# Optimization experiments

Measured on AMD Instinct MI355X. Metric: run time of the kernel, lower is better.

The kernel has to match this reference:

```python
import jax, jax.numpy as jnp
import numpy as np

EMB = 1024
HID = 2048
HEADS = 16
CONV = 4


def causal_conv1d(z, w):
    # z: [B, H, T], w: [H, K] depthwise causal conv
    K = w.shape[1]
    T = z.shape[-1]
    zp = jnp.pad(z, ((0, 0), (0, 0), (K - 1, 0)))  # [B, H, T+K-1]
    out = jnp.zeros_like(z)
    for k in range(K):  # tiny fixed loop over taps (K<=4)
        out = out + w[None, :, k, None] * jax.lax.dynamic_slice_in_dim(zp, k, T, axis=2)
    return out


def linear_scan(a, b):
    # h_t = a_t * h_{t-1} + b_t along last axis; associative scan
    def combine(c1, c2):
        a1, b1 = c1
        a2, b2 = c2
        return a1 * a2, a2 * b1 + b2
    _, h = jax.lax.associative_scan(combine, (a, b), axis=-1)
    return h


def setup_inputs() -> dict:
    key = jax.random.key(0)
    k1, k2, k3, k4 = jax.random.split(key, 4)
    x = jax.random.normal(k1, (4, 2048, EMB), dtype=jnp.float32)
    w1 = jax.random.normal(k2, (3 * HID, EMB), dtype=jnp.float32) * (EMB ** -0.5)
    w2 = jax.random.normal(k3, (EMB, HID), dtype=jnp.float32) * (HID ** -0.5)
    conv_weight = jax.random.normal(k4, (HID, CONV), dtype=jnp.float32) * (CONV ** -0.5)
    return {"x": x, "w1": w1, "w2": w2, "conv_weight": conv_weight}


def reference(x, w1, w2, conv_weight):
    bsz, seq_len, _ = x.shape
    head_dim = HID // HEADS
    y = jnp.einsum("bse,he->bsh", x, w1)  # [B, S, 3*HID]
    out1, z, h = jnp.split(y, 3, axis=-1)
    z = jnp.swapaxes(z, 1, 2)  # [B, HID, S]
    h = jnp.swapaxes(h, 1, 2)
    z = causal_conv1d(z, conv_weight)
    z = jax.nn.sigmoid(z)
    z = z.reshape(bsz * HEADS, head_dim, seq_len)
    h = h.reshape(bsz * HEADS, head_dim, seq_len)
    h = linear_scan(1.0 - z, z * h)
    out2 = jnp.swapaxes(h.reshape(bsz, HID, seq_len), 1, 2)  # [B, S, HID]
    out = jax.nn.silu(out1) * out2
    return jnp.einsum("bsh,eh->bse", out, w2)
```

## Files before the change

kernel.cpp:

```cpp
#include <hip/hip_runtime.h>
#include <cstdint>

#define EMB 1024
#define HID 2048
#define BATCH 4
#define SEQ 2048
#define MROWS (BATCH * SEQ)
#define N1 (3 * HID)
#define K1 EMB
#define N2 EMB
#define K2 HID

#define NX (MROWS * EMB)
#define NW1 (N1 * K1)
#define NW2 (N2 * K2)

#define SEG 32
#define SLEN (SEQ / SEG)

typedef unsigned short ushort_t;
typedef __bf16 bf16x8 __attribute__((ext_vector_type(8)));
typedef float f32x4 __attribute__((ext_vector_type(4)));
typedef ushort_t us4 __attribute__((ext_vector_type(4)));

__device__ __forceinline__ ushort_t f2bf(float f) {
    uint32_t u = __builtin_bit_cast(uint32_t, f);
    u += 0x7fffu + ((u >> 16) & 1u);
    return (ushort_t)(u >> 16);
}
__device__ __forceinline__ float bf2f(ushort_t h) {
    uint32_t u = ((uint32_t)h) << 16;
    return __builtin_bit_cast(float, u);
}
__device__ __forceinline__ float bflo(uint32_t v) {
    return __builtin_bit_cast(float, v << 16);
}
__device__ __forceinline__ float bfhi(uint32_t v) {
    return __builtin_bit_cast(float, v & 0xffff0000u);
}
__device__ __forceinline__ float sigm(float x) {
    return 1.f / (1.f + __expf(-x));
}

__device__ __forceinline__ void gload_lds16(const ushort_t* g, const ushort_t* l) {
    __builtin_amdgcn_global_load_lds(
        (const __attribute__((address_space(1))) void*)(uintptr_t)(g),
        (__attribute__((address_space(3))) void*)(uint32_t)(uintptr_t)(l),
        16, 0, 0);
}

__global__ __launch_bounds__(256) void cvt_kernel(
    const float* __restrict__ x, const float* __restrict__ w1,
    const float* __restrict__ w2, ushort_t* __restrict__ xb,
    ushort_t* __restrict__ w1b, ushort_t* __restrict__ w2b) {
    const int i = (blockIdx.x * 256 + threadIdx.x) * 4;
    const float* s;
    ushort_t* d;
    if (i < NX) {
        s = x + i; d = xb + i;
    } else if (i < NX + NW1) {
        s = w1 + (i - NX); d = w1b + (i - NX);
    } else {
        s = w2 + (i - NX - NW1); d = w2b + (i - NX - NW1);
    }
    const float4 v = *(const float4*)s;
    us4 o;
    o.x = f2bf(v.x); o.y = f2bf(v.y); o.z = f2bf(v.z); o.w = f2bf(v.w);
    *(us4*)d = o;
}

template <bool OUT_BF16>
__global__ __launch_bounds__(256) void gemm_bt(
    const ushort_t* __restrict__ A, const ushort_t* __restrict__ B,
    void* __restrict__ Cv, int M, int N, int K) {
    __shared__ ushort_t sA[128 * 32];
    __shared__ ushort_t sB[128 * 32];

    const int tid  = threadIdx.x;
    const int lane = tid & 63;
    const int wave = tid >> 6;
    const int quad = lane >> 4;
    const int l16  = lane & 15;
    const long tm0 = (long)blockIdx.y * 128;
    const long tn0 = (long)blockIdx.x * 128;
    const int wm = (wave & 1) * 64;
    const int wn = (wave >> 1) * 64;

    f32x4 acc[4][4] = {};

    const int ar0 = tid >> 2;
    const int ar1 = (tid + 256) >> 2;
    const int kq  = (tid & 3) ^ ((ar0 >> 1) & 3);
    const int ac  = kq * 8;
    const ushort_t* gA = A + (size_t)tm0 * K;
    const ushort_t* gB = B + (size_t)tn0 * K;
    ushort_t* lb0 = &sA[0] + wave * 512;
    ushort_t* lb1 = &sA[0] + 2048 + wave * 512;
    ushort_t* lb2 = &sB[0] + wave * 512;
    ushort_t* lb3 = &sB[0] + 2048 + wave * 512;

    const int rsw = (l16 >> 1) & 3;
    const int aoff = (quad ^ rsw) * 8 + l16 * 32;

    for (int k0 = 0; k0 < K; k0 += 32) {
        __syncthreads();
        gload_lds16(gA + (size_t)ar0 * K + k0 + ac, lb0);
        gload_lds16(gA + (size_t)ar1 * K + k0 + ac, lb1);
        gload_lds16(gB + (size_t)ar0 * K + k0 + ac, lb2);
        gload_lds16(gB + (size_t)ar1 * K + k0 + ac, lb3);
        __syncthreads();

        bf16x8 af[4], bfr[4];
#pragma unroll
        for (int i = 0; i < 4; ++i)
            af[i] = *(const bf16x8*)&sA[(wm + i * 16) * 32 + aoff];
#pragma unroll
        for (int j = 0; j < 4; ++j)
            bfr[j] = *(const bf16x8*)&sB[(wn + j * 16) * 32 + aoff];
#pragma unroll
        for (int i = 0; i < 4; ++i)
#pragma unroll
            for (int j = 0; j < 4; ++j)
                acc[i][j] = __builtin_amdgcn_mfma_f32_16x16x32_bf16(
                    af[i], bfr[j], acc[i][j], 0, 0, 0);
    }

#pragma unroll
    for (int i = 0; i < 4; ++i) {
        const long row0 = tm0 + wm + i * 16 + quad * 4;
#pragma unroll
        for (int j = 0; j < 4; ++j) {
            const long col = tn0 + wn + j * 16 + l16;
#pragma unroll
            for (int r = 0; r < 4; ++r) {
                if constexpr (OUT_BF16) {
                    ((ushort_t*)Cv)[(size_t)(row0 + r) * N + col] = f2bf(acc[i][j][r]);
                } else {
                    ((float*)Cv)[(size_t)(row0 + r) * N + col] = acc[i][j][r];
                }
            }
        }
    }
}

__global__ __launch_bounds__(256) void scan_part1(
    const ushort_t* __restrict__ y, const float* __restrict__ cw,
    float* __restrict__ Ag, float* __restrict__ Bg) {
    const int gid = blockIdx.x * 256 + threadIdx.x;
    const int ch  = (gid & 1023) * 2;
    const int bs  = gid >> 10;
    const int b   = bs >> 5;
    const int seg = bs & 31;
    const int t0  = seg * SLEN;
    const size_t rowbase = (size_t)b * SEQ;
    const ushort_t* yz = y + 2048 + ch;
    const ushort_t* yh = y + 4096 + ch;

    float w[2][4];
#pragma unroll
    for (int c = 0; c < 2; ++c)
#pragma unroll
        for (int k = 0; k < 4; ++k) w[c][k] = cw[(ch + c) * 4 + k];

    auto ld2 = [&](const ushort_t* p, int t) -> uint32_t {
        return *(const uint32_t*)(p + (rowbase + (size_t)t) * 6144);
    };
    auto zpair = [&](int t, float* out) {
        if (t < 0) { out[0] = 0.f; out[1] = 0.f; }
        else { uint32_t v = ld2(yz, t); out[0] = bflo(v); out[1] = bfhi(v); }
    };

    float z1[2], z2[2], z3[2], A[2] = {1.f, 1.f}, Bv[2] = {0.f, 0.f};
    zpair(t0 - 1, z1); zpair(t0 - 2, z2); zpair(t0 - 3, z3);

#pragma unroll 4
    for (int t = t0; t < t0 + SLEN; ++t) {
        const uint32_t vz = ld2(yz, t);
        const uint32_t vh = ld2(yh, t);
        const float zr[2] = {bflo(vz), bfhi(vz)};
        const float hr[2] = {bflo(vh), bfhi(vh)};
#pragma unroll
        for (int c = 0; c < 2; ++c) {
            const float cv = w[c][0] * z3[c] + w[c][1] * z2[c] +
                             w[c][2] * z1[c] + w[c][3] * zr[c];
            const float s = sigm(cv);
            z3[c] = z2[c]; z2[c] = z1[c]; z1[c] = zr[c];
            const float a = 1.f - s;
            A[c] *= a;
            Bv[c] = a * Bv[c] + s * hr[c];
        }
    }
    const size_t idx = ((size_t)b * SEG + seg) * HID + ch;
    *(float2*)&Ag[idx] = make_float2(A[0], A[1]);
    *(float2*)&Bg[idx] = make_float2(Bv[0], Bv[1]);
}

__global__ __launch_bounds__(256) void scan_part2(
    const float* __restrict__ Ag, const float* __restrict__ Bg,
    float* __restrict__ Cr) {
    const int gid = blockIdx.x * 256 + threadIdx.x;
    const int b  = gid >> 11;
    const int ch = gid & 2047;
    float carry = 0.f;
#pragma unroll
    for (int s = 0; s < SEG; ++s) {
        const size_t idx = ((size_t)b * SEG + s) * HID + ch;
        Cr[idx] = carry;
        carry = Ag[idx] * carry + Bg[idx];
    }
}

__global__ __launch_bounds__(256) void scan_part3(
    const ushort_t* __restrict__ y, const float* __restrict__ cw,
    const float* __restrict__ Cr, ushort_t* __restrict__ u) {
    const int gid = blockIdx.x * 256 + threadIdx.x;
    const int ch  = (gid & 1023) * 2;
    const int bs  = gid >> 10;
    const int b   = bs >> 5;
    const int seg = bs & 31;
    const int t0  = seg * SLEN;
    const size_t rowbase = (size_t)b * SEQ;
    const ushort_t* yo = y + ch;
    const ushort_t* yz = y + 2048 + ch;
    const ushort_t* yh = y + 4096 + ch;

    float w[2][4];
#pragma unroll
    for (int c = 0; c < 2; ++c)
#pragma unroll
        for (int k = 0; k < 4; ++k) w[c][k] = cw[(ch + c) * 4 + k];

    auto ld2 = [&](const ushort_t* p, int t) -> uint32_t {
        return *(const uint32_t*)(p + (rowbase + (size_t)t) * 6144);
    };
    auto zpair = [&](int t, float* out) {
        if (t < 0) { out[0] = 0.f; out[1] = 0.f; }
        else { uint32_t v = ld2(yz, t); out[0] = bflo(v); out[1] = bfhi(v); }
    };

    const size_t cidx = ((size_t)b * SEG + seg) * HID + ch;
    float h[2] = {Cr[cidx], Cr[cidx + 1]};
    float z1[2], z2[2], z3[2];
    zpair(t0 - 1, z1); zpair(t0 - 2, z2); zpair(t0 - 3, z3);

#pragma unroll 4
    for (int t = t0; t < t0 + SLEN; ++t) {
        const uint32_t vz = ld2(yz, t);
        const uint32_t vh = ld2(yh, t);
        const uint32_t vo = ld2(yo, t);
        const float zr[2] = {bflo(vz), bfhi(vz)};
        const float hr[2] = {bflo(vh), bfhi(vh)};
        const float o1[2] = {bflo(vo), bfhi(vo)};
        ushort_t res[2];
#pragma unroll
        for (int c = 0; c < 2; ++c) {
            const float cv = w[c][0] * z3[c] + w[c][1] * z2[c] +
                             w[c][2] * z1[c] + w[c][3] * zr[c];
            const float s = sigm(cv);
            z3[c] = z2[c]; z2[c] = z1[c]; z1[c] = zr[c];
            h[c] = (1.f - s) * h[c] + s * hr[c];
            const float sil = o1[c] * sigm(o1[c]);
            res[c] = f2bf(sil * h[c]);
        }
        *(uint32_t*)&u[(rowbase + (size_t)t) * (size_t)HID + ch] =
            (uint32_t)res[0] | ((uint32_t)res[1] << 16);
    }
}

extern "C" void kernel_launch(void* const* d_in, const int* in_sizes, int n_in,
                              void* d_out, int out_size, void* d_ws, size_t ws_size,
                              hipStream_t stream) {
    const float* x  = (const float*)d_in[0];
    const float* w1 = (const float*)d_in[1];
    const float* w2 = (const float*)d_in[2];
    const float* cw = (const float*)d_in[3];
    char* ws = (char*)d_ws;

    ushort_t* xb  = (ushort_t*)(ws);
    ushort_t* w1b = (ushort_t*)(ws + (size_t)16777216);
    ushort_t* w2b = (ushort_t*)(ws + (size_t)29360128);
    ushort_t* y   = (ushort_t*)(ws + (size_t)33554432);
    ushort_t* u   = (ushort_t*)(ws + (size_t)134217728);
    float* Ag = (float*)(ws);
    float* Bg = (float*)(ws + (size_t)1048576);
    float* Cr = (float*)(ws + (size_t)2097152);
    float* out = (float*)d_out;

    cvt_kernel<<<16384, 256, 0, stream>>>(x, w1, w2, xb, w1b, w2b);
    gemm_bt<true><<<dim3(N1 / 128, MROWS / 128), 256, 0, stream>>>(
        xb, w1b, (void*)y, MROWS, N1, K1);
    scan_part1<<<512, 256, 0, stream>>>(y, cw, Ag, Bg);
    scan_part2<<<32, 256, 0, stream>>>(Ag, Bg, Cr);
    scan_part3<<<512, 256, 0, stream>>>(y, cw, Cr, u);
    gemm_bt<false><<<dim3(N2 / 128, MROWS / 128), 256, 0, stream>>>(
        u, w2b, (void*)out, MROWS, N2, K2);
}
```

Baseline: 358.5 us.

## Fuse three scan kernels into one cooperative kernel with register-cached inputs

Replaces the three-pass chunked scan (local reduce, carry propagation, apply) with a single cooperative kernel that uses a grid-wide sync. Each thread keeps its 64 z/h bf16 pairs in registers, so the second pass no longer re-reads them from global memory. After the sync, each thread rebuilds its own carry by walking the earlier segments' (A,B) pairs. This removes two launches, the Cr buffer and the duplicate z/h reads, but costs 128 extra registers per thread, a grid barrier and redundant carry work per segment. Co-residency of all 512 blocks is also required.

```diff
diff --git a/kernel.cpp b/kernel.cpp
--- a/kernel.cpp
+++ b/kernel.cpp
@@ -1,5 +1,8 @@
 #include <hip/hip_runtime.h>
+#include <hip/hip_cooperative_groups.h>
 #include <cstdint>
+
+namespace cg = cooperative_groups;
 
 #define EMB 1024
 #define HID 2048
@@ -143,76 +146,10 @@
     }
 }
 
-__global__ __launch_bounds__(256) void scan_part1(
+__global__ void scan_coop(
     const ushort_t* __restrict__ y, const float* __restrict__ cw,
-    float* __restrict__ Ag, float* __restrict__ Bg) {
-    const int gid = blockIdx.x * 256 + threadIdx.x;
-    const int ch  = (gid & 1023) * 2;
-    const int bs  = gid >> 10;
-    const int b   = bs >> 5;
-    const int seg = bs & 31;
-    const int t0  = seg * SLEN;
-    const size_t rowbase = (size_t)b * SEQ;
-    const ushort_t* yz = y + 2048 + ch;
-    const ushort_t* yh = y + 4096 + ch;
-
-    float w[2][4];
-#pragma unroll
-    for (int c = 0; c < 2; ++c)
-#pragma unroll
-        for (int k = 0; k < 4; ++k) w[c][k] = cw[(ch + c) * 4 + k];
-
-    auto ld2 = [&](const ushort_t* p, int t) -> uint32_t {
-        return *(const uint32_t*)(p + (rowbase + (size_t)t) * 6144);
-    };
-    auto zpair = [&](int t, float* out) {
-        if (t < 0) { out[0] = 0.f; out[1] = 0.f; }
-        else { uint32_t v = ld2(yz, t); out[0] = bflo(v); out[1] = bfhi(v); }
-    };
-
-    float z1[2], z2[2], z3[2], A[2] = {1.f, 1.f}, Bv[2] = {0.f, 0.f};
-    zpair(t0 - 1, z1); zpair(t0 - 2, z2); zpair(t0 - 3, z3);
-
-#pragma unroll 4
-    for (int t = t0; t < t0 + SLEN; ++t) {
-        const uint32_t vz = ld2(yz, t);
-        const uint32_t vh = ld2(yh, t);
-        const float zr[2] = {bflo(vz), bfhi(vz)};
-        const float hr[2] = {bflo(vh), bfhi(vh)};
-#pragma unroll
-        for (int c = 0; c < 2; ++c) {
-            const float cv = w[c][0] * z3[c] + w[c][1] * z2[c] +
-                             w[c][2] * z1[c] + w[c][3] * zr[c];
-            const float s = sigm(cv);
-            z3[c] = z2[c]; z2[c] = z1[c]; z1[c] = zr[c];
-            const float a = 1.f - s;
-            A[c] *= a;
-            Bv[c] = a * Bv[c] + s * hr[c];
-        }
-    }
-    const size_t idx = ((size_t)b * SEG + seg) * HID + ch;
-    *(float2*)&Ag[idx] = make_float2(A[0], A[1]);
-    *(float2*)&Bg[idx] = make_float2(Bv[0], Bv[1]);
-}
-
-__global__ __launch_bounds__(256) void scan_part2(
-    const float* __restrict__ Ag, const float* __restrict__ Bg,
-    float* __restrict__ Cr) {
-    const int gid = blockIdx.x * 256 + threadIdx.x;
-    const int b  = gid >> 11;
-    const int ch = gid & 2047;
-    float carry = 0.f;
-#pragma unroll
-    for (int s = 0; s < SEG; ++s) {
-        const size_t idx = ((size_t)b * SEG + s) * HID + ch;
-        Cr[idx] = carry;
-        carry = Ag[idx] * carry + Bg[idx];
-    }
-}
-
-__global__ __launch_bounds__(256) void scan_part3(
-    const ushort_t* __restrict__ y, const float* __restrict__ cw,
-    const float* __restrict__ Cr, ushort_t* __restrict__ u) {
+    float* __restrict__ Ag, float* __restrict__ Bg,
+    ushort_t* __restrict__ u) {
     const int gid = blockIdx.x * 256 + threadIdx.x;
     const int ch  = (gid & 1023) * 2;
     const int bs  = gid >> 10;
@@ -238,18 +175,55 @@
         else { uint32_t v = ld2(yz, t); out[0] = bflo(v); out[1] = bfhi(v); }
     };
 
-    const size_t cidx = ((size_t)b * SEG + seg) * HID + ch;
-    float h[2] = {Cr[cidx], Cr[cidx + 1]};
-    float z1[2], z2[2], z3[2];
-    zpair(t0 - 1, z1); zpair(t0 - 2, z2); zpair(t0 - 3, z3);
-
-#pragma unroll 4
-    for (int t = t0; t < t0 + SLEN; ++t) {
-        const uint32_t vz = ld2(yz, t);
-        const uint32_t vh = ld2(yh, t);
-        const uint32_t vo = ld2(yo, t);
-        const float zr[2] = {bflo(vz), bfhi(vz)};
-        const float hr[2] = {bflo(vh), bfhi(vh)};
+    uint32_t za[SLEN], ha[SLEN];
+#pragma unroll
+    for (int t = 0; t < SLEN; ++t) {
+        za[t] = ld2(yz, t0 + t);
+        ha[t] = ld2(yh, t0 + t);
+    }
+    float zw1[2], zw2[2], zw3[2];
+    zpair(t0 - 1, zw1); zpair(t0 - 2, zw2); zpair(t0 - 3, zw3);
+
+    float z1[2] = {zw1[0], zw1[1]}, z2[2] = {zw2[0], zw2[1]}, z3[2] = {zw3[0], zw3[1]};
+    float A[2] = {1.f, 1.f}, Bv[2] = {0.f, 0.f};
+#pragma unroll
+    for (int t = 0; t < SLEN; ++t) {
+        const float zr[2] = {bflo(za[t]), bfhi(za[t])};
+        const float hr[2] = {bflo(ha[t]), bfhi(ha[t])};
+#pragma unroll
+        for (int c = 0; c < 2; ++c) {
+            const float cv = w[c][0] * z3[c] + w[c][1] * z2[c] +
+                             w[c][2] * z1[c] + w[c][3] * zr[c];
+            const float s = sigm(cv);
+            z3[c] = z2[c]; z2[c] = z1[c]; z1[c] = zr[c];
+            const float a = 1.f - s;
+            A[c] *= a;
+            Bv[c] = a * Bv[c] + s * hr[c];
+        }
+    }
+    const size_t aidx = ((size_t)b * SEG + seg) * HID + ch;
+    *(float2*)&Ag[aidx] = make_float2(A[0], A[1]);
+    *(float2*)&Bg[aidx] = make_float2(Bv[0], Bv[1]);
+
+    cg::this_grid().sync();
+
+    float h[2] = {0.f, 0.f};
+    for (int s = 0; s < seg; ++s) {
+        const size_t idx = ((size_t)b * SEG + s) * HID + ch;
+        const float2 a2 = *(const float2*)&Ag[idx];
+        const float2 b2 = *(const float2*)&Bg[idx];
+        h[0] = a2.x * h[0] + b2.x;
+        h[1] = a2.y * h[1] + b2.y;
+    }
+
+    z1[0] = zw1[0]; z1[1] = zw1[1];
+    z2[0] = zw2[0]; z2[1] = zw2[1];
+    z3[0] = zw3[0]; z3[1] = zw3[1];
+#pragma unroll
+    for (int t = 0; t < SLEN; ++t) {
+        const uint32_t vo = ld2(yo, t0 + t);
+        const float zr[2] = {bflo(za[t]), bfhi(za[t])};
+        const float hr[2] = {bflo(ha[t]), bfhi(ha[t])};
         const float o1[2] = {bflo(vo), bfhi(vo)};
         ushort_t res[2];
 #pragma unroll
@@ -262,7 +236,7 @@
             const float sil = o1[c] * sigm(o1[c]);
             res[c] = f2bf(sil * h[c]);
         }
-        *(uint32_t*)&u[(rowbase + (size_t)t) * (size_t)HID + ch] =
+        *(uint32_t*)&u[(rowbase + (size_t)(t0 + t)) * (size_t)HID + ch] =
             (uint32_t)res[0] | ((uint32_t)res[1] << 16);
     }
 }
@@ -283,15 +257,21 @@
     ushort_t* u   = (ushort_t*)(ws + (size_t)134217728);
     float* Ag = (float*)(ws);
     float* Bg = (float*)(ws + (size_t)1048576);
-    float* Cr = (float*)(ws + (size_t)2097152);
     float* out = (float*)d_out;
 
     cvt_kernel<<<16384, 256, 0, stream>>>(x, w1, w2, xb, w1b, w2b);
     gemm_bt<true><<<dim3(N1 / 128, MROWS / 128), 256, 0, stream>>>(
         xb, w1b, (void*)y, MROWS, N1, K1);
-    scan_part1<<<512, 256, 0, stream>>>(y, cw, Ag, Bg);
-    scan_part2<<<32, 256, 0, stream>>>(Ag, Bg, Cr);
-    scan_part3<<<512, 256, 0, stream>>>(y, cw, Cr, u);
+    {
+        const ushort_t* ya = y;
+        const float* cwa = cw;
+        float* Aga = Ag;
+        float* Bga = Bg;
+        ushort_t* ua = u;
+        void* args[] = {(void*)&ya, (void*)&cwa, (void*)&Aga, (void*)&Bga, (void*)&ua};
+        hipLaunchCooperativeKernel((void*)scan_coop, dim3(512), dim3(256),
+                                   args, 0, stream);
+    }
     gemm_bt<false><<<dim3(N2 / 128, MROWS / 128), 256, 0, stream>>>(
         u, w2b, (void*)out, MROWS, N2, K2);
 }
```

Result: slower. 690.8 us (+92.7%).
